# Kernel optimization log

Hardware: AMD Instinct MI355X
Metric: run time of the kernel (lower is better)

Reference implementation:

```python
import jax, jax.numpy as jnp
import numpy as np

B, G, S, C = 64, 2048, 64, 3


def setup_inputs() -> dict:
    key = jax.random.key(0)
    k1, k2 = jax.random.split(key)
    neighbor = jax.random.normal(k1, (B, G, S, C), dtype=jnp.float32)
    center = jax.random.normal(k2, (B, G, C), dtype=jnp.float32)
    return {"neighbor": neighbor, "center": center}


def _disambiguate_vector_directions(lps, vecs):
    # lps: [B,G,S,3] local points; vecs: [B,G,3] candidate axes.
    knn = lps.shape[2]
    proj = jnp.sum(vecs[:, :, None, :] * lps, axis=3)                 # [B,G,S]
    n_pos = jnp.sum((proj > 0).astype(jnp.float32), axis=2, keepdims=True)  # [B,G,1]
    flip = (n_pos < 0.5 * knn).astype(jnp.float32)
    return (1.0 - 2.0 * flip) * vecs


def reference(neighbor, center):
    # neighbor: [B,G,S,3] (C==3 path -> axis1/axis2 both PCA)
    pos = neighbor[..., 0:3]
    # Distance-based weights for weighted PCA covariance.
    norms = jnp.linalg.norm(pos, axis=3, keepdims=True)               # [B,G,S,1]
    max_norms = jnp.max(norms, axis=2, keepdims=True)                 # [B,G,1,1]
    w = max_norms - norms
    w = w / (jnp.sum(w, axis=2, keepdims=True) + 1e-6)
    scaled_pos = 100.0 * pos
    # Weighted covariance: [B,G,3,3]
    covs = jnp.einsum('bgsk,bgsl->bgkl', w * scaled_pos, scaled_pos)
    # Symmetric 3x3 eigendecomposition, eigenvalues ascending, eigenvectors as columns
    # (same convention as pytorch3d symeig3x3; signs fixed by disambiguation below).
    _, eigvec = jnp.linalg.eigh(covs)                                 # [B,G,3,3]
    z_axis = _disambiguate_vector_directions(pos, eigvec[:, :, :, 0])  # smallest-eig
    x_axis = _disambiguate_vector_directions(pos, eigvec[:, :, :, 2])  # largest-eig
    y_axis = jnp.cross(z_axis, x_axis)                                # [B,G,3]
    lrfs = jnp.stack((z_axis, y_axis, x_axis), axis=3)                # [B,G,3,3] (columns)
    # Rotate local points into the LRF: batched [S,3] x [3,3]
    rot_neighbor = jnp.einsum('bgsc,bgcd->bgsd', pos, lrfs)           # [B,G,S,3]
    return (rot_neighbor, lrfs)
```

## Files before the change

kernel.cpp:

```cpp
#include <hip/hip_runtime.h>
#include <math.h>


__device__ __forceinline__ float slapy2_(float x, float y) {
    _Pragma("clang fp contract(off)")
    float xa = fabsf(x), ya = fabsf(y);
    float w = fmaxf(xa, ya), z = fminf(xa, ya);
    if (z == 0.0f) return w;
    float t = z / w;
    return w * sqrtf(1.0f + t * t);
}

__device__ __forceinline__ void slartg_(float f, float g,
                                        float &c, float &s, float &r) {
    _Pragma("clang fp contract(off)")
    if (g == 0.0f) { c = 1.0f; s = 0.0f; r = f; return; }
    if (f == 0.0f) { c = 0.0f; s = (g >= 0.0f) ? 1.0f : -1.0f; r = fabsf(g); return; }
    float d = sqrtf(f * f + g * g);
    float p = 1.0f / d;
    c = fabsf(f) * p;
    s = g * ((f >= 0.0f) ? p : -p);
    r = (f >= 0.0f) ? d : -d;
}

__device__ __forceinline__ void slaev2_(float a, float b, float cc,
                                        float &rt1, float &rt2,
                                        float &cs1, float &sn1) {
    _Pragma("clang fp contract(off)")
    float sm = a + cc, df = a - cc;
    float adf = fabsf(df);
    float tb = b + b;
    float ab = fabsf(tb);
    float acmx, acmn;
    if (fabsf(a) > fabsf(cc)) { acmx = a; acmn = cc; } else { acmx = cc; acmn = a; }
    float rt;
    if (adf > ab)      { float t = ab / adf; rt = adf * sqrtf(1.0f + t * t); }
    else if (adf < ab) { float t = adf / ab; rt = ab * sqrtf(1.0f + t * t); }
    else                rt = ab * sqrtf(2.0f);
    int sgn1;
    if (sm < 0.0f)      { rt1 = 0.5f * (sm - rt); sgn1 = -1; rt2 = (acmx / rt1) * acmn - (b / rt1) * b; }
    else if (sm > 0.0f) { rt1 = 0.5f * (sm + rt); sgn1 =  1; rt2 = (acmx / rt1) * acmn - (b / rt1) * b; }
    else                { rt1 = 0.5f * rt; rt2 = -0.5f * rt; sgn1 = 1; }
    int sgn2;
    float cs;
    if (df >= 0.0f) { cs = df + rt; sgn2 = 1; } else { cs = df - rt; sgn2 = -1; }
    float acs = fabsf(cs);
    if (acs > ab) {
        float ct = -tb / cs;
        sn1 = 1.0f / sqrtf(1.0f + ct * ct);
        cs1 = ct * sn1;
    } else {
        if (ab == 0.0f) { cs1 = 1.0f; sn1 = 0.0f; }
        else {
            float tn = -cs / tb;
            cs1 = 1.0f / sqrtf(1.0f + tn * tn);
            sn1 = tn * cs1;
        }
    }
    if (sgn1 == sgn2) { float tn = cs1; cs1 = -sn1; sn1 = tn; }
}

__device__ __forceinline__ float getd3(int i, float d1, float d2, float d3) {
    return (i == 1) ? d1 : ((i == 2) ? d2 : d3);
}
__device__ __forceinline__ void setd3(int i, float v, float &d1, float &d2, float &d3) {
    d1 = (i == 1) ? v : d1;
    d2 = (i == 2) ? v : d2;
    d3 = (i == 3) ? v : d3;
}
__device__ __forceinline__ float gete2(int i, float e1, float e2) {
    return (i == 1) ? e1 : e2;
}
__device__ __forceinline__ void sete2(int i, float v, float &e1, float &e2) {
    e1 = (i == 1) ? v : e1;
    e2 = (i == 2) ? v : e2;
}

__device__ __forceinline__ void zrot3r(int j, float ctemp, float stemp,
                                       float &z11, float &z12, float &z13,
                                       float &z21, float &z22, float &z23,
                                       float &z31, float &z32, float &z33) {
    _Pragma("clang fp contract(off)")
    if (j == 1) {
        { float t = z12; z12 = (ctemp * t) - (stemp * z11); z11 = (stemp * t) + (ctemp * z11); }
        { float t = z22; z22 = (ctemp * t) - (stemp * z21); z21 = (stemp * t) + (ctemp * z21); }
        { float t = z32; z32 = (ctemp * t) - (stemp * z31); z31 = (stemp * t) + (ctemp * z31); }
    } else {
        { float t = z13; z13 = (ctemp * t) - (stemp * z12); z12 = (stemp * t) + (ctemp * z12); }
        { float t = z23; z23 = (ctemp * t) - (stemp * z22); z22 = (stemp * t) + (ctemp * z22); }
        { float t = z33; z33 = (ctemp * t) - (stemp * z32); z32 = (stemp * t) + (ctemp * z32); }
    }
}

__device__ __forceinline__ void ssteqr3_reg(
        float &d1_, float &d2_, float &d3_, float &e1_, float &e2_,
        float &z11, float &z12, float &z13,
        float &z21, float &z22, float &z23,
        float &z31, float &z32, float &z33) {
    _Pragma("clang fp contract(off)")
    const float EPS    = 5.9604644775390625e-8f;
    const float EPS2   = EPS * EPS;
    const float SAFMIN = 1.17549435e-38f;
    const int n = 3, nmaxit = 3 * 30;
    int jtot = 0, l1 = 1;

#define GD(i)      getd3((i), d1_, d2_, d3_)
#define SD(i, v)   setd3((i), (v), d1_, d2_, d3_)
#define GE(i)      gete2((i), e1_, e2_)
#define SE(i, v)   sete2((i), (v), e1_, e2_)
#define ZR(j, c, s) zrot3r((j), (c), (s), z11, z12, z13, z21, z22, z23, z31, z32, z33)

    while (true) {
        if (l1 > n) break;
        if (l1 > 1) SE(l1 - 1, 0.0f);
        int m = n;
        for (int mm = l1; mm <= n - 1; ++mm) {
            float tst = fabsf(GE(mm));
            if (tst == 0.0f) { m = mm; break; }
            if (tst <= (sqrtf(fabsf(GD(mm))) * sqrtf(fabsf(GD(mm + 1)))) * EPS) {
                SE(mm, 0.0f); m = mm; break;
            }
        }
        int l = l1, lsv = l, lend = m, lendsv = lend;
        l1 = m + 1;
        if (lend == l) continue;
        if (fabsf(GD(lend)) < fabsf(GD(l))) { lend = lsv; l = lendsv; }

        if (lend > l) {
            while (true) {
                m = lend;
                if (l != lend) {
                    for (int mm = l; mm <= lend - 1; ++mm) {
                        float em = GE(mm);
                        float tst = em * em;
                        if (tst <= (EPS2 * fabsf(GD(mm))) * fabsf(GD(mm + 1)) + SAFMIN) { m = mm; break; }
                    }
                }
                if (m < lend) SE(m, 0.0f);
                float p = GD(l);
                if (m == l) {
                    SD(l, p); ++l;
                    if (l <= lend) continue;
                    break;
                }
                if (m == l + 1) {
                    float rt1, rt2, c, s;
                    slaev2_(GD(l), GE(l), GD(l + 1), rt1, rt2, c, s);
                    ZR(l, c, s);
                    SD(l, rt1); SD(l + 1, rt2); SE(l, 0.0f);
                    l += 2;
                    if (l <= lend) continue;
                    break;
                }
                if (jtot == nmaxit) break;
                ++jtot;
                {
                    float el = GE(l);
                    float g = (GD(l + 1) - p) / (2.0f * el);
                    float r = slapy2_(g, 1.0f);
                    g = GD(m) - p + el / (g + ((g >= 0.0f) ? r : -r));
                    float s = 1.0f, c = 1.0f;
                    p = 0.0f;
                    for (int i = m - 1; i >= l; --i) {
                        float ei = GE(i);
                        float f = s * ei;
                        float b = c * ei;
                        slartg_(g, f, c, s, r);
                        if (i != m - 1) SE(i + 1, r);
                        g = GD(i + 1) - p;
                        float r2 = ((GD(i) - g) * s) + ((2.0f * c) * b);
                        p = s * r2;
                        SD(i + 1, g + p);
                        g = (c * r2) - b;
                        ZR(i, c, -s);
                    }
                    SD(l, GD(l) - p);
                    SE(l, g);
                }
            }
        } else if (lend < l) {
            while (true) {
                m = lend;
                if (l != lend) {
                    for (int mm = l; mm >= lend + 1; --mm) {
                        float em = GE(mm - 1);
                        float tst = em * em;
                        if (tst <= (EPS2 * fabsf(GD(mm))) * fabsf(GD(mm - 1)) + SAFMIN) { m = mm; break; }
                    }
                }
                if (m > lend) SE(m - 1, 0.0f);
                float p = GD(l);
                if (m == l) {
                    SD(l, p); --l;
                    if (l >= lend) continue;
                    break;
                }
                if (m == l - 1) {
                    float rt1, rt2, c, s;
                    slaev2_(GD(l - 1), GE(l - 1), GD(l), rt1, rt2, c, s);
                    ZR(l - 1, c, s);
                    SD(l - 1, rt1); SD(l, rt2); SE(l - 1, 0.0f);
                    l -= 2;
                    if (l >= lend) continue;
                    break;
                }
                if (jtot == nmaxit) break;
                ++jtot;
                {
                    float el = GE(l - 1);
                    float g = (GD(l - 1) - p) / (2.0f * el);
                    float r = slapy2_(g, 1.0f);
                    g = GD(m) - p + el / (g + ((g >= 0.0f) ? r : -r));
                    float s = 1.0f, c = 1.0f;
                    p = 0.0f;
                    for (int i = m; i <= l - 1; ++i) {
                        float ei = GE(i);
                        float f = s * ei;
                        float b = c * ei;
                        slartg_(g, f, c, s, r);
                        if (i != m) SE(i - 1, r);
                        g = GD(i) - p;
                        float r2 = ((GD(i + 1) - g) * s) + ((2.0f * c) * b);
                        p = s * r2;
                        SD(i, g + p);
                        g = (c * r2) - b;
                        ZR(i, c, s);
                    }
                    SD(l, GD(l) - p);
                    SE(l - 1, g);
                }
            }
        }
    }
    {
        int k = 1; float p = d1_;
        if (d2_ < p) { k = 2; p = d2_; }
        if (d3_ < p) { k = 3; p = d3_; }
        if (k == 2) {
            d2_ = d1_; d1_ = p;
            float t;
            t = z11; z11 = z12; z12 = t;
            t = z21; z21 = z22; z22 = t;
            t = z31; z31 = z32; z32 = t;
        } else if (k == 3) {
            d3_ = d1_; d1_ = p;
            float t;
            t = z11; z11 = z13; z13 = t;
            t = z21; z21 = z23; z23 = t;
            t = z31; z31 = z33; z33 = t;
        }
        if (d3_ < d2_) {
            float t = d2_; d2_ = d3_; d3_ = t;
            t = z12; z12 = z13; z13 = t;
            t = z22; z22 = z23; z23 = t;
            t = z32; z32 = z33; z33 = t;
        }
    }
#undef GD
#undef SD
#undef GE
#undef SE
#undef ZR
}

__device__ __forceinline__ float nrm3_(float x, float y, float z) {
    _Pragma("clang fp contract(off)")
    float t = (x * x) + (y * y);
    t = t + (z * z);
    return sqrtf(t);
}

__device__ __forceinline__ void covstep(float px, float py, float pz, float nrm,
                                        float mx, float denom,
                                        float &c00, float &c10, float &c20,
                                        float &c11, float &c21, float &c22) {
    _Pragma("clang fp contract(off)")
    const float w  = mx - nrm;
    const float wq = w / denom;
    const float spx = 100.0f * px, spy = 100.0f * py, spz = 100.0f * pz;
    const float ax = wq * spx, ay = wq * spy, az = wq * spz;
    c00 = c00 + (ax * spx);
    c10 = c10 + (ay * spx);
    c20 = c20 + (az * spx);
    c11 = c11 + (ay * spy);
    c21 = c21 + (az * spy);
    c22 = c22 + (az * spz);
}

__device__ __forceinline__ void projstep(float px, float py, float pz,
                                         float zv0, float zv1, float zv2,
                                         float xv0, float xv1, float xv2,
                                         int &cz, int &cx) {
    _Pragma("clang fp contract(off)")
    const float pjz = ((zv0 * px) + (zv1 * py)) + (zv2 * pz);
    const float pjx = ((xv0 * px) + (xv1 * py)) + (xv2 * pz);
    cz += (pjz > 0.0f) ? 1 : 0;
    cx += (pjx > 0.0f) ? 1 : 0;
}

__device__ __forceinline__ void rotstep(float px, float py, float pz,
                                        float zv0, float zv1, float zv2,
                                        float yv0, float yv1, float yv2,
                                        float xv0, float xv1, float xv2,
                                        float &ra, float &rb, float &rc) {
    _Pragma("clang fp contract(off)")
    ra = ((px * zv0) + (py * zv1)) + (pz * zv2);
    rb = ((px * yv0) + (py * yv1)) + (pz * yv2);
    rc = ((px * xv0) + (py * xv1)) + (pz * xv2);
}

__global__ __launch_bounds__(64, 2) void lrf_kernel(const float* __restrict__ nbr,
                                                    float* __restrict__ rot,
                                                    float* __restrict__ lrf) {
    _Pragma("clang fp contract(off)")
    __shared__ float nlds[64 * 65];
    const int tid = threadIdx.x;
    const int g = (blockIdx.x << 6) + tid;
    const float4* __restrict__ p4 = reinterpret_cast<const float4*>(nbr) + g * 48;
    const int tb = tid * 65;

    float mx = -3.402823466e+38f;
#pragma unroll 4
    for (int q = 0; q < 16; ++q) {
        const float4 v0 = p4[q * 3 + 0];
        const float4 v1 = p4[q * 3 + 1];
        const float4 v2 = p4[q * 3 + 2];
        const float n0 = nrm3_(v0.x, v0.y, v0.z);
        const float n1 = nrm3_(v0.w, v1.x, v1.y);
        const float n2 = nrm3_(v1.z, v1.w, v2.x);
        const float n3 = nrm3_(v2.y, v2.z, v2.w);
        nlds[tb + 4 * q + 0] = n0;
        nlds[tb + 4 * q + 1] = n1;
        nlds[tb + 4 * q + 2] = n2;
        nlds[tb + 4 * q + 3] = n3;
        mx = fmaxf(mx, fmaxf(fmaxf(n0, n1), fmaxf(n2, n3)));
    }

    float r0 = 0.0f, r1 = 0.0f, r2 = 0.0f, r3 = 0.0f,
          r4 = 0.0f, r5 = 0.0f, r6 = 0.0f, r7 = 0.0f;
#pragma unroll
    for (int k = 0; k < 8; ++k) {
        const int b = tb + 8 * k;
        r0 = r0 + (mx - nlds[b + 0]);
        r1 = r1 + (mx - nlds[b + 1]);
        r2 = r2 + (mx - nlds[b + 2]);
        r3 = r3 + (mx - nlds[b + 3]);
        r4 = r4 + (mx - nlds[b + 4]);
        r5 = r5 + (mx - nlds[b + 5]);
        r6 = r6 + (mx - nlds[b + 6]);
        r7 = r7 + (mx - nlds[b + 7]);
    }
    const float ws = ((r0 + r1) + (r2 + r3)) + ((r4 + r5) + (r6 + r7));
    const float denom = ws + 1e-6f;

    float c00 = 0.0f, c10 = 0.0f, c20 = 0.0f, c11 = 0.0f, c21 = 0.0f, c22 = 0.0f;
#pragma unroll 4
    for (int q = 0; q < 16; ++q) {
        const float4 v0 = p4[q * 3 + 0];
        const float4 v1 = p4[q * 3 + 1];
        const float4 v2 = p4[q * 3 + 2];
        covstep(v0.x, v0.y, v0.z, nlds[tb + 4 * q + 0], mx, denom, c00, c10, c20, c11, c21, c22);
        covstep(v0.w, v1.x, v1.y, nlds[tb + 4 * q + 1], mx, denom, c00, c10, c20, c11, c21, c22);
        covstep(v1.z, v1.w, v2.x, nlds[tb + 4 * q + 2], mx, denom, c00, c10, c20, c11, c21, c22);
        covstep(v2.y, v2.z, v2.w, nlds[tb + 4 * q + 3], mx, denom, c00, c10, c20, c11, c21, c22);
    }

    const float a11 = c00, a21 = c10, a31 = c20, a22 = c11, a32 = c21, a33 = c22;

    float taui, v2h, e1q, d2q, d3q, e2q;
    const float xnorm = fabsf(a31);
    if (xnorm == 0.0f) {
        taui = 0.0f; v2h = a31; e1q = a21; d2q = a22; e2q = a32; d3q = a33;
    } else {
        const float beta = -copysignf(slapy2_(a21, xnorm), a21);
        taui = (beta - a21) / beta;
        const float rcp = 1.0f / (a21 - beta);
        v2h = a31 * rcp;
        e1q = beta;
        float x1 = taui * a22;
        float x2 = taui * a32;
        const float temp2 = a32 * v2h;
        x1 = x1 + (taui * temp2);
        const float t1v = taui * v2h;
        x2 = x2 + (t1v * a33);
        const float dt = x1 + (x2 * v2h);
        const float alpha_c = (-0.5f * taui) * dt;
        const float w1 = x1 + alpha_c;
        const float w2 = x2 + (alpha_c * v2h);
        d2q = (a22 - w1) - w1;
        e2q = (a32 - (v2h * w1)) - w2;
        d3q = (a33 - (v2h * w2)) - (w2 * v2h);
    }

    float d1_ = a11, d2_ = d2q, d3_ = d3q, e1_ = e1q, e2_ = e2q;
    float z11 = 1.0f, z12 = 0.0f, z13 = 0.0f;
    float z21 = 0.0f, z22 = 1.0f, z23 = 0.0f;
    float z31 = 0.0f, z32 = 0.0f, z33 = 1.0f;
    ssteqr3_reg(d1_, d2_, d3_, e1_, e2_,
                z11, z12, z13, z21, z22, z23, z31, z32, z33);

    float zv0, zv1, zv2, xv0, xv1, xv2;
    {
        const float u2 = z21, u3 = z31;
        zv0 = z11;
        if (taui != 0.0f) {
            const float wj = u2 + (u3 * v2h);
            const float pj = taui * wj;
            zv1 = u2 - pj;
            zv2 = u3 - (v2h * pj);
        } else { zv1 = u2; zv2 = u3; }
    }
    {
        const float u2 = z23, u3 = z33;
        xv0 = z13;
        if (taui != 0.0f) {
            const float wj = u2 + (u3 * v2h);
            const float pj = taui * wj;
            xv1 = u2 - pj;
            xv2 = u3 - (v2h * pj);
        } else { xv1 = u2; xv2 = u3; }
    }

    int cz = 0, cx = 0;
#pragma unroll 4
    for (int q = 0; q < 16; ++q) {
        const float4 v0 = p4[q * 3 + 0];
        const float4 v1 = p4[q * 3 + 1];
        const float4 v2 = p4[q * 3 + 2];
        projstep(v0.x, v0.y, v0.z, zv0, zv1, zv2, xv0, xv1, xv2, cz, cx);
        projstep(v0.w, v1.x, v1.y, zv0, zv1, zv2, xv0, xv1, xv2, cz, cx);
        projstep(v1.z, v1.w, v2.x, zv0, zv1, zv2, xv0, xv1, xv2, cz, cx);
        projstep(v2.y, v2.z, v2.w, zv0, zv1, zv2, xv0, xv1, xv2, cz, cx);
    }
    if (cz < 32) { zv0 = -zv0; zv1 = -zv1; zv2 = -zv2; }
    if (cx < 32) { xv0 = -xv0; xv1 = -xv1; xv2 = -xv2; }

    const float yv0 = (zv1 * xv2) - (zv2 * xv1);
    const float yv1 = (zv2 * xv0) - (zv0 * xv2);
    const float yv2 = (zv0 * xv1) - (zv1 * xv0);

    float4* __restrict__ o4 = reinterpret_cast<float4*>(rot) + g * 48;
#pragma unroll 4
    for (int q = 0; q < 16; ++q) {
        const float4 v0 = p4[q * 3 + 0];
        const float4 v1 = p4[q * 3 + 1];
        const float4 v2 = p4[q * 3 + 2];
        float r0a, r0b, r0c, r1a, r1b, r1c, r2a, r2b, r2c, r3a, r3b, r3c;
        rotstep(v0.x, v0.y, v0.z, zv0, zv1, zv2, yv0, yv1, yv2, xv0, xv1, xv2, r0a, r0b, r0c);
        rotstep(v0.w, v1.x, v1.y, zv0, zv1, zv2, yv0, yv1, yv2, xv0, xv1, xv2, r1a, r1b, r1c);
        rotstep(v1.z, v1.w, v2.x, zv0, zv1, zv2, yv0, yv1, yv2, xv0, xv1, xv2, r2a, r2b, r2c);
        rotstep(v2.y, v2.z, v2.w, zv0, zv1, zv2, yv0, yv1, yv2, xv0, xv1, xv2, r3a, r3b, r3c);
        float4 o0, o1, o2;
        o0.x = r0a; o0.y = r0b; o0.z = r0c; o0.w = r1a;
        o1.x = r1b; o1.y = r1c; o1.z = r2a; o1.w = r2b;
        o2.x = r2c; o2.y = r3a; o2.z = r3b; o2.w = r3c;
        o4[q * 3 + 0] = o0;
        o4[q * 3 + 1] = o1;
        o4[q * 3 + 2] = o2;
    }

    float* __restrict__ lp = lrf + g * 9;
    lp[0] = zv0; lp[1] = yv0; lp[2] = xv0;
    lp[3] = zv1; lp[4] = yv1; lp[5] = xv1;
    lp[6] = zv2; lp[7] = yv2; lp[8] = xv2;
}

extern "C" void kernel_launch(void* const* d_in, const int* in_sizes, int n_in,
                              void* d_out, int out_size, void* d_ws, size_t ws_size,
                              hipStream_t stream) {
    const float* neighbor = (const float*)d_in[0];
    float* rot = (float*)d_out;
    float* lrf = (float*)d_out + (long long)64 * 2048 * 64 * 3;

    lrf_kernel<<<dim3(2048), dim3(64), 0, stream>>>(neighbor, rot, lrf);
}
```

Before: 299.8 us.

## Split each group across four lanes with shuffle reductions and fused sign-flip

Each neighbourhood group is now handled by four consecutive lanes instead of one, with 256-thread blocks. Each lane computes norms for its quarter of the points, and max, weight sum and sign counts are combined with xor-shuffles. Projection and rotation are fused into one pass that writes unsigned rotations to registers and applies the signs afterwards, so the neighbour data is read one fewer time. The covariance accumulation and the 3x3 eigen solve are still done redundantly by all four lanes. The aim is to raise wave-level parallelism and latency hiding in a kernel that previously launched very few waves per CU.

```diff
diff --git a/kernel.cpp b/kernel.cpp
--- a/kernel.cpp
+++ b/kernel.cpp
@@ -270,13 +270,10 @@
     return sqrtf(t);
 }
 
-__device__ __forceinline__ void covstep(float px, float py, float pz, float nrm,
-                                        float mx, float denom,
+__device__ __forceinline__ void covstep(float px, float py, float pz, float wq,
                                         float &c00, float &c10, float &c20,
                                         float &c11, float &c21, float &c22) {
     _Pragma("clang fp contract(off)")
-    const float w  = mx - nrm;
-    const float wq = w / denom;
     const float spx = 100.0f * px, spy = 100.0f * py, spz = 100.0f * pz;
     const float ax = wq * spx, ay = wq * spy, az = wq * spz;
     c00 = c00 + (ax * spx);
@@ -287,17 +284,6 @@
     c22 = c22 + (az * spz);
 }
 
-__device__ __forceinline__ void projstep(float px, float py, float pz,
-                                         float zv0, float zv1, float zv2,
-                                         float xv0, float xv1, float xv2,
-                                         int &cz, int &cx) {
-    _Pragma("clang fp contract(off)")
-    const float pjz = ((zv0 * px) + (zv1 * py)) + (zv2 * pz);
-    const float pjx = ((xv0 * px) + (xv1 * py)) + (xv2 * pz);
-    cz += (pjz > 0.0f) ? 1 : 0;
-    cx += (pjx > 0.0f) ? 1 : 0;
-}
-
 __device__ __forceinline__ void rotstep(float px, float py, float pz,
                                         float zv0, float zv1, float zv2,
                                         float yv0, float yv1, float yv2,
@@ -309,19 +295,25 @@
     rc = ((px * xv0) + (py * xv1)) + (pz * xv2);
 }
 
-__global__ __launch_bounds__(64, 2) void lrf_kernel(const float* __restrict__ nbr,
-                                                    float* __restrict__ rot,
-                                                    float* __restrict__ lrf) {
-    _Pragma("clang fp contract(off)")
-    __shared__ float nlds[64 * 65];
+__global__ __launch_bounds__(256, 4) void lrf_kernel(const float* __restrict__ nbr,
+                                                     float* __restrict__ rot,
+                                                     float* __restrict__ lrf) {
+    _Pragma("clang fp contract(off)")
+    __shared__ float wql[64 * 65];
     const int tid = threadIdx.x;
-    const int g = (blockIdx.x << 6) + tid;
-    const float4* __restrict__ p4 = reinterpret_cast<const float4*>(nbr) + g * 48;
-    const int tb = tid * 65;
+    const int gl  = tid >> 2;
+    const int k   = tid & 3;
+    const int g   = (blockIdx.x << 6) + gl;
+    const int lbase = gl * 65;
+
+    const float4* __restrict__ p4 = reinterpret_cast<const float4*>(nbr)
+                                    + (long long)g * 48 + k * 12;
+    const float4* __restrict__ q4 = reinterpret_cast<const float4*>(nbr)
+                                    + (long long)g * 48;
 
     float mx = -3.402823466e+38f;
-#pragma unroll 4
-    for (int q = 0; q < 16; ++q) {
+#pragma unroll
+    for (int q = 0; q < 4; ++q) {
         const float4 v0 = p4[q * 3 + 0];
         const float4 v1 = p4[q * 3 + 1];
         const float4 v2 = p4[q * 3 + 2];
@@ -329,40 +321,56 @@
         const float n1 = nrm3_(v0.w, v1.x, v1.y);
         const float n2 = nrm3_(v1.z, v1.w, v2.x);
         const float n3 = nrm3_(v2.y, v2.z, v2.w);
-        nlds[tb + 4 * q + 0] = n0;
-        nlds[tb + 4 * q + 1] = n1;
-        nlds[tb + 4 * q + 2] = n2;
-        nlds[tb + 4 * q + 3] = n3;
+        const int b = lbase + 16 * k + 4 * q;
+        wql[b + 0] = n0;
+        wql[b + 1] = n1;
+        wql[b + 2] = n2;
+        wql[b + 3] = n3;
         mx = fmaxf(mx, fmaxf(fmaxf(n0, n1), fmaxf(n2, n3)));
     }
-
-    float r0 = 0.0f, r1 = 0.0f, r2 = 0.0f, r3 = 0.0f,
-          r4 = 0.0f, r5 = 0.0f, r6 = 0.0f, r7 = 0.0f;
+    mx = fmaxf(mx, __shfl_xor(mx, 1, 64));
+    mx = fmaxf(mx, __shfl_xor(mx, 2, 64));
+    __builtin_amdgcn_wave_barrier();
+    asm volatile("" ::: "memory");
+
+    float r0_ = 0.0f, r1_ = 0.0f;
+    {
+        const int j0 = lbase + 2 * k;
 #pragma unroll
-    for (int k = 0; k < 8; ++k) {
-        const int b = tb + 8 * k;
-        r0 = r0 + (mx - nlds[b + 0]);
-        r1 = r1 + (mx - nlds[b + 1]);
-        r2 = r2 + (mx - nlds[b + 2]);
-        r3 = r3 + (mx - nlds[b + 3]);
-        r4 = r4 + (mx - nlds[b + 4]);
-        r5 = r5 + (mx - nlds[b + 5]);
-        r6 = r6 + (mx - nlds[b + 6]);
-        r7 = r7 + (mx - nlds[b + 7]);
-    }
-    const float ws = ((r0 + r1) + (r2 + r3)) + ((r4 + r5) + (r6 + r7));
+        for (int t = 0; t < 8; ++t) {
+            r0_ = r0_ + (mx - wql[j0 + 8 * t + 0]);
+            r1_ = r1_ + (mx - wql[j0 + 8 * t + 1]);
+        }
+    }
+    const float A_ = r0_ + r1_;
+    const float B_ = A_ + __shfl_xor(A_, 1, 64);
+    const float ws = B_ + __shfl_xor(B_, 2, 64);
     const float denom = ws + 1e-6f;
+    asm volatile("" ::: "memory");
+
+#pragma unroll
+    for (int i = 0; i < 16; ++i) {
+        const int idx = lbase + 16 * k + i;
+        const float nv = wql[idx];
+        wql[idx] = (mx - nv) / denom;
+    }
+    __builtin_amdgcn_wave_barrier();
+    asm volatile("" ::: "memory");
 
     float c00 = 0.0f, c10 = 0.0f, c20 = 0.0f, c11 = 0.0f, c21 = 0.0f, c22 = 0.0f;
 #pragma unroll 4
     for (int q = 0; q < 16; ++q) {
-        const float4 v0 = p4[q * 3 + 0];
-        const float4 v1 = p4[q * 3 + 1];
-        const float4 v2 = p4[q * 3 + 2];
-        covstep(v0.x, v0.y, v0.z, nlds[tb + 4 * q + 0], mx, denom, c00, c10, c20, c11, c21, c22);
-        covstep(v0.w, v1.x, v1.y, nlds[tb + 4 * q + 1], mx, denom, c00, c10, c20, c11, c21, c22);
-        covstep(v1.z, v1.w, v2.x, nlds[tb + 4 * q + 2], mx, denom, c00, c10, c20, c11, c21, c22);
-        covstep(v2.y, v2.z, v2.w, nlds[tb + 4 * q + 3], mx, denom, c00, c10, c20, c11, c21, c22);
+        const float4 v0 = q4[q * 3 + 0];
+        const float4 v1 = q4[q * 3 + 1];
+        const float4 v2 = q4[q * 3 + 2];
+        const float w0 = wql[lbase + 4 * q + 0];
+        const float w1 = wql[lbase + 4 * q + 1];
+        const float w2 = wql[lbase + 4 * q + 2];
+        const float w3 = wql[lbase + 4 * q + 3];
+        covstep(v0.x, v0.y, v0.z, w0, c00, c10, c20, c11, c21, c22);
+        covstep(v0.w, v1.x, v1.y, w1, c00, c10, c20, c11, c21, c22);
+        covstep(v1.z, v1.w, v2.x, w2, c00, c10, c20, c11, c21, c22);
+        covstep(v2.y, v2.z, v2.w, w3, c00, c10, c20, c11, c21, c22);
     }
 
     const float a11 = c00, a21 = c10, a31 = c20, a22 = c11, a32 = c21, a33 = c22;
@@ -421,48 +429,70 @@
         } else { xv1 = u2; xv2 = u3; }
     }
 
+    const float yv0 = (zv1 * xv2) - (zv2 * xv1);
+    const float yv1 = (zv2 * xv0) - (zv0 * xv2);
+    const float yv2 = (zv0 * xv1) - (zv1 * xv0);
+
+    float fr[48];
     int cz = 0, cx = 0;
-#pragma unroll 4
-    for (int q = 0; q < 16; ++q) {
+#pragma unroll
+    for (int q = 0; q < 4; ++q) {
         const float4 v0 = p4[q * 3 + 0];
         const float4 v1 = p4[q * 3 + 1];
         const float4 v2 = p4[q * 3 + 2];
-        projstep(v0.x, v0.y, v0.z, zv0, zv1, zv2, xv0, xv1, xv2, cz, cx);
-        projstep(v0.w, v1.x, v1.y, zv0, zv1, zv2, xv0, xv1, xv2, cz, cx);
-        projstep(v1.z, v1.w, v2.x, zv0, zv1, zv2, xv0, xv1, xv2, cz, cx);
-        projstep(v2.y, v2.z, v2.w, zv0, zv1, zv2, xv0, xv1, xv2, cz, cx);
-    }
-    if (cz < 32) { zv0 = -zv0; zv1 = -zv1; zv2 = -zv2; }
-    if (cx < 32) { xv0 = -xv0; xv1 = -xv1; xv2 = -xv2; }
-
-    const float yv0 = (zv1 * xv2) - (zv2 * xv1);
-    const float yv1 = (zv2 * xv0) - (zv0 * xv2);
-    const float yv2 = (zv0 * xv1) - (zv1 * xv0);
-
-    float4* __restrict__ o4 = reinterpret_cast<float4*>(rot) + g * 48;
-#pragma unroll 4
-    for (int q = 0; q < 16; ++q) {
-        const float4 v0 = p4[q * 3 + 0];
-        const float4 v1 = p4[q * 3 + 1];
-        const float4 v2 = p4[q * 3 + 2];
-        float r0a, r0b, r0c, r1a, r1b, r1c, r2a, r2b, r2c, r3a, r3b, r3c;
-        rotstep(v0.x, v0.y, v0.z, zv0, zv1, zv2, yv0, yv1, yv2, xv0, xv1, xv2, r0a, r0b, r0c);
-        rotstep(v0.w, v1.x, v1.y, zv0, zv1, zv2, yv0, yv1, yv2, xv0, xv1, xv2, r1a, r1b, r1c);
-        rotstep(v1.z, v1.w, v2.x, zv0, zv1, zv2, yv0, yv1, yv2, xv0, xv1, xv2, r2a, r2b, r2c);
-        rotstep(v2.y, v2.z, v2.w, zv0, zv1, zv2, yv0, yv1, yv2, xv0, xv1, xv2, r3a, r3b, r3c);
-        float4 o0, o1, o2;
-        o0.x = r0a; o0.y = r0b; o0.z = r0c; o0.w = r1a;
-        o1.x = r1b; o1.y = r1c; o1.z = r2a; o1.w = r2b;
-        o2.x = r2c; o2.y = r3a; o2.z = r3b; o2.w = r3c;
-        o4[q * 3 + 0] = o0;
-        o4[q * 3 + 1] = o1;
-        o4[q * 3 + 2] = o2;
-    }
-
-    float* __restrict__ lp = lrf + g * 9;
-    lp[0] = zv0; lp[1] = yv0; lp[2] = xv0;
-    lp[3] = zv1; lp[4] = yv1; lp[5] = xv1;
-    lp[6] = zv2; lp[7] = yv2; lp[8] = xv2;
+        rotstep(v0.x, v0.y, v0.z, zv0, zv1, zv2, yv0, yv1, yv2, xv0, xv1, xv2,
+                fr[12 * q + 0], fr[12 * q + 1], fr[12 * q + 2]);
+        rotstep(v0.w, v1.x, v1.y, zv0, zv1, zv2, yv0, yv1, yv2, xv0, xv1, xv2,
+                fr[12 * q + 3], fr[12 * q + 4], fr[12 * q + 5]);
+        rotstep(v1.z, v1.w, v2.x, zv0, zv1, zv2, yv0, yv1, yv2, xv0, xv1, xv2,
+                fr[12 * q + 6], fr[12 * q + 7], fr[12 * q + 8]);
+        rotstep(v2.y, v2.z, v2.w, zv0, zv1, zv2, yv0, yv1, yv2, xv0, xv1, xv2,
+                fr[12 * q + 9], fr[12 * q + 10], fr[12 * q + 11]);
+        cz += (fr[12 * q + 0] > 0.0f) ? 1 : 0;
+        cz += (fr[12 * q + 3] > 0.0f) ? 1 : 0;
+        cz += (fr[12 * q + 6] > 0.0f) ? 1 : 0;
+        cz += (fr[12 * q + 9] > 0.0f) ? 1 : 0;
+        cx += (fr[12 * q + 2] > 0.0f) ? 1 : 0;
+        cx += (fr[12 * q + 5] > 0.0f) ? 1 : 0;
+        cx += (fr[12 * q + 8] > 0.0f) ? 1 : 0;
+        cx += (fr[12 * q + 11] > 0.0f) ? 1 : 0;
+    }
+    cz += __shfl_xor(cz, 1, 64);
+    cz += __shfl_xor(cz, 2, 64);
+    cx += __shfl_xor(cx, 1, 64);
+    cx += __shfl_xor(cx, 2, 64);
+    const float sz = (cz < 32) ? -1.0f : 1.0f;
+    const float sx = (cx < 32) ? -1.0f : 1.0f;
+    const float sy = sz * sx;
+
+#pragma unroll
+    for (int f = 0; f < 48; ++f) {
+        const int c = f % 3;
+        const float sc = (c == 0) ? sz : ((c == 1) ? sy : sx);
+        fr[f] = fr[f] * sc;
+    }
+
+    float4* __restrict__ o4 = reinterpret_cast<float4*>(rot)
+                              + (long long)g * 48 + k * 12;
+#pragma unroll
+    for (int q = 0; q < 12; ++q) {
+        float4 t;
+        t.x = fr[4 * q + 0];
+        t.y = fr[4 * q + 1];
+        t.z = fr[4 * q + 2];
+        t.w = fr[4 * q + 3];
+        o4[q] = t;
+    }
+
+    if (k < 3) {
+        const float zc = ((k == 0) ? zv0 : ((k == 1) ? zv1 : zv2)) * sz;
+        const float yc = ((k == 0) ? yv0 : ((k == 1) ? yv1 : yv2)) * sy;
+        const float xc = ((k == 0) ? xv0 : ((k == 1) ? xv1 : xv2)) * sx;
+        float* __restrict__ lp = lrf + (long long)g * 9 + 3 * k;
+        lp[0] = zc;
+        lp[1] = yc;
+        lp[2] = xc;
+    }
 }
 
 extern "C" void kernel_launch(void* const* d_in, const int* in_sizes, int n_in,
@@ -472,5 +502,5 @@
     float* rot = (float*)d_out;
     float* lrf = (float*)d_out + (long long)64 * 2048 * 64 * 3;
 
-    lrf_kernel<<<dim3(2048), dim3(64), 0, stream>>>(neighbor, rot, lrf);
-}
+    lrf_kernel<<<dim3(2048), dim3(256), 0, stream>>>(neighbor, rot, lrf);
+}
```

Result: faster. 274.8 us (-8.3%).
